# Performance work log

Hardware: AMD Instinct MI355X
Metric: run time of the kernel (lower is better)

## Reference

```python
import jax, jax.numpy as jnp
import numpy as np

N, G, S = 51200, 128, 400  # nodes, graphs, nodes-per-graph
E, IN, H, OUT = 819200, 128, 128, 10


def _graph_conv(x, src, dst, W_rel, b_rel, W_root):
    # PyG GraphConv (aggr='add'): lin_rel(sum_{j->i} x_j) + lin_root(x_i)
    agg = jax.ops.segment_sum(x[src], dst, num_segments=N)  # [N, d]
    return agg @ W_rel + b_rel + x @ W_root


def _mixup(x, lam, perm):
    return x * lam + (1.0 - lam) * x[perm]


def setup_inputs() -> dict:
    key = jax.random.key(0)
    ks = jax.random.split(key, 12)
    rng = np.random.default_rng(0)

    x0 = jax.random.normal(ks[0], (N, IN), dtype=jnp.float32)
    edge_index = jax.random.randint(ks[1], (2, E), 0, N, dtype=jnp.int64)
    lam = jax.random.uniform(ks[2], (1,), dtype=jnp.float32)
    ptr = jnp.arange(0, N + 1, S, dtype=jnp.int64)            # [G+1]
    batch = jnp.repeat(jnp.arange(G, dtype=jnp.int64), S)     # [N]

    def seg_perm():
        return jnp.asarray(np.concatenate(
            [g * S + rng.permutation(S) for g in range(G)]), dtype=jnp.int64)

    perm1, perm2, perm3 = seg_perm(), seg_perm(), seg_perm()

    def lin(k, fan_in, fan_out):
        bound = 1.0 / np.sqrt(fan_in)
        return jax.random.uniform(k, (fan_in, fan_out), jnp.float32, -bound, bound)

    params = {
        'W1_rel': lin(ks[3], IN, H), 'b1_rel': jnp.zeros((H,), jnp.float32),
        'W1_root': lin(ks[4], IN, H),
        'W2_rel': lin(ks[5], H, H), 'b2_rel': jnp.zeros((H,), jnp.float32),
        'W2_root': lin(ks[6], H, H),
        'W_lin': lin(ks[7], H, OUT), 'b_lin': jnp.zeros((OUT,), jnp.float32),
    }
    return dict(x0=x0, edge_index=edge_index, lam=lam, ptr=ptr, batch=batch,
                perm1=perm1, perm2=perm2, perm3=perm3, **params)


def reference(x0, edge_index, lam, ptr, batch, perm1, perm2, perm3,
              W1_rel, b1_rel, W1_root, W2_rel, b2_rel, W2_root, W_lin, b_lin):
    src, dst = edge_index[0], edge_index[1]
    l = lam[0]

    x1 = jax.nn.relu(_graph_conv(x0, src, dst, W1_rel, b1_rel, W1_root))
    x1 = _mixup(x1, l, perm1)  # dropout p=0.4 is identity in eval mode

    x2 = jax.nn.relu(_graph_conv(x1, src, dst, W2_rel, b2_rel, W2_root))
    x2 = _mixup(x2, l, perm2)

    # NOTE: original forward reuses conv2 for the third layer (conv3 unused)
    x3 = jax.nn.relu(_graph_conv(x2, src, dst, W2_rel, b2_rel, W2_root))
    x3 = _mixup(x3, l, perm3)

    pooled = jax.ops.segment_sum(x3, batch, num_segments=G)  # [G, H]
    logits = pooled @ W_lin + b_lin                          # [G, OUT]
    return jax.nn.log_softmax(logits, axis=-1)
```

## Files before the change

### kernel.cpp

```cpp
#include <hip/hip_runtime.h>

#define N_NODES 51200
#define N_EDGES 819200
#define HDIM 128
#define AK 256
#define NGRAPH 128
#define SEG 400
#define NOUT 10
#define SLOT 64

#define HISTW (N_NODES / 4)
#define NBLK 200
#define EPB (N_EDGES / NBLK)
#define SEGS 8
#define BPSEG (NBLK / SEGS)

typedef unsigned short ushort_t;
typedef unsigned int uint_t;
typedef __attribute__((ext_vector_type(8))) short bf16x8;
typedef __attribute__((ext_vector_type(16))) float f32x16;

static __device__ __forceinline__ unsigned short f2bf(float f) {
    unsigned int u = __float_as_uint(f);
    unsigned int r = (u + 0x7fffu + ((u >> 16) & 1u)) >> 16;
    return (unsigned short)r;
}
static __device__ __forceinline__ float bf2f(unsigned short h) {
    return __uint_as_float(((unsigned int)h) << 16);
}


__global__ void k_prep(const float* __restrict__ x, ushort_t* __restrict__ Abuf,
                       const float* __restrict__ W1rel, const float* __restrict__ W1root,
                       const float* __restrict__ W2rel, const float* __restrict__ W2root,
                       ushort_t* __restrict__ Wfrag1, ushort_t* __restrict__ Wfrag2,
                       float* __restrict__ pooled) {
    int b = blockIdx.x;
    if (b < 6400) {
        int idx = b * 256 + threadIdx.x;
        int row = idx >> 5;
        int c4 = (idx & 31) * 4;
        float4 v = *(const float4*)(x + (size_t)row * HDIM + c4);
        ushort4 h;
        h.x = f2bf(v.x); h.y = f2bf(v.y); h.z = f2bf(v.z); h.w = f2bf(v.w);
        *(ushort4*)(Abuf + (size_t)row * AK + HDIM + c4) = h;
    } else if (b < 6656) {
        int w2 = (b >= 6528);
        int tid = (b - (w2 ? 6528 : 6400)) * 256 + threadIdx.x;
        const float* Wrel  = w2 ? W2rel : W1rel;
        const float* Wroot = w2 ? W2root : W1root;
        ushort_t* dstF     = w2 ? Wfrag2 : Wfrag1;
        int j = tid & 7;
        int l = (tid >> 3) & 63;
        int s = (tid >> 9) & 15;
        int t = tid >> 13;
        int k = 16 * s + (l >> 5) * 8 + j;
        int n = 32 * t + (l & 31);
        float v = (k < HDIM) ? Wrel[(size_t)k * HDIM + n]
                             : Wroot[(size_t)(k - HDIM) * HDIM + n];
        dstF[tid] = f2bf(v);
    } else {
        int i = (b - 6656) * 256 + threadIdx.x;
        pooled[i] = 0.f;
    }
}


__global__ __launch_bounds__(256) void k_count(const int* __restrict__ dst,
                                               uint_t* __restrict__ bh) {
    __shared__ uint_t hist[HISTW];
    int b = blockIdx.x, tid = threadIdx.x;
    for (int i = tid; i < HISTW; i += 256) hist[i] = 0u;
    __syncthreads();
    const int4* d4 = (const int4*)dst + b * (EPB / 4);
#pragma unroll
    for (int p = 0; p < 4; ++p) {
        int4 d = d4[p * 256 + tid];
        atomicAdd(&hist[((uint_t)d.x) >> 2], 1u << ((d.x & 3) * 8));
        atomicAdd(&hist[((uint_t)d.y) >> 2], 1u << ((d.y & 3) * 8));
        atomicAdd(&hist[((uint_t)d.z) >> 2], 1u << ((d.z & 3) * 8));
        atomicAdd(&hist[((uint_t)d.w) >> 2], 1u << ((d.w & 3) * 8));
    }
    __syncthreads();
    for (int i = tid; i < HISTW; i += 256) bh[(size_t)b * HISTW + i] = hist[i];
}


__global__ __launch_bounds__(256) void k_prefix(uint_t* __restrict__ bh,
                                                int* __restrict__ cnt) {
    __shared__ uint_t segsum[SEGS][32];
    int ci = threadIdx.x & 31;
    int seg = threadIdx.x >> 5;
    int c = blockIdx.x * 32 + ci;
    uint_t v[BPSEG];
    uint_t sum = 0;
#pragma unroll
    for (int k = 0; k < BPSEG; ++k) {
        v[k] = bh[(size_t)(seg * BPSEG + k) * HISTW + c];
        sum += v[k];
    }
    segsum[seg][ci] = sum;
    __syncthreads();
    uint_t run = 0;
    for (int s = 0; s < seg; ++s) run += segsum[s][ci];
#pragma unroll
    for (int k = 0; k < BPSEG; ++k) {
        bh[(size_t)(seg * BPSEG + k) * HISTW + c] = run;
        run += v[k];
    }
    if (seg == SEGS - 1) {
        int4 o;
        o.x = (int)(run & 0xffu);
        o.y = (int)((run >> 8) & 0xffu);
        o.z = (int)((run >> 16) & 0xffu);
        o.w = (int)((run >> 24) & 0xffu);
        *(int4*)(cnt + 4 * c) = o;
    }
}


__global__ __launch_bounds__(256) void k_place(const int* __restrict__ src,
                                               const int* __restrict__ dst,
                                               const uint_t* __restrict__ bh,
                                               ushort_t* __restrict__ col2) {
    __shared__ uint_t hist[HISTW];
    int b = blockIdx.x, tid = threadIdx.x;
    for (int i = tid; i < HISTW; i += 256) hist[i] = bh[(size_t)b * HISTW + i];
    __syncthreads();
    const int4* d4 = (const int4*)dst + b * (EPB / 4);
    const int4* s4 = (const int4*)src + b * (EPB / 4);
#pragma unroll
    for (int p = 0; p < 4; ++p) {
        int4 d = d4[p * 256 + tid];
        int4 s = s4[p * 256 + tid];
#define PLACE1(dd, ss)                                                        \
        do {                                                                  \
            uint_t w = (uint_t)(dd);                                          \
            int sh = (int)(w & 3u) * 8;                                       \
            uint_t old = atomicAdd(&hist[w >> 2], 1u << sh);                  \
            col2[(size_t)w * SLOT + ((old >> sh) & 0xffu)] = (ushort_t)(ss);  \
        } while (0)
        PLACE1(d.x, s.x);
        PLACE1(d.y, s.y);
        PLACE1(d.z, s.z);
        PLACE1(d.w, s.w);
#undef PLACE1
    }
}


__global__ __launch_bounds__(256) void k_aggregate(ushort_t* __restrict__ Abuf,
                                                   const int* __restrict__ cnt,
                                                   const ushort_t* __restrict__ col) {
    int wave = threadIdx.x >> 6;
    int lane = threadIdx.x & 63;
    int il = lane & 15;
    int qe = lane >> 4;
    int node = blockIdx.x * 4 + wave;
    int beg = node * SLOT;
    int end = beg + cnt[node];

    const ushort_t* xsrc = Abuf + HDIM + (size_t)il * 8;

    float a[4][8];
#pragma unroll
    for (int j = 0; j < 4; ++j)
#pragma unroll
        for (int k = 0; k < 8; ++k) a[j][k] = 0.f;

    int e = beg;
    for (; e + 16 <= end; e += 16) {
        int c[4];
#pragma unroll
        for (int j = 0; j < 4; ++j) c[j] = (int)col[e + 4 * j + qe];
#pragma unroll
        for (int j = 0; j < 4; ++j) {
            uint4 v = *(const uint4*)(xsrc + (size_t)c[j] * AK);
            a[j][0] += __uint_as_float(v.x << 16);
            a[j][1] += __uint_as_float(v.x & 0xffff0000u);
            a[j][2] += __uint_as_float(v.y << 16);
            a[j][3] += __uint_as_float(v.y & 0xffff0000u);
            a[j][4] += __uint_as_float(v.z << 16);
            a[j][5] += __uint_as_float(v.z & 0xffff0000u);
            a[j][6] += __uint_as_float(v.w << 16);
            a[j][7] += __uint_as_float(v.w & 0xffff0000u);
        }
    }
    for (; e + 4 <= end; e += 4) {
        int c = (int)col[e + qe];
        uint4 v = *(const uint4*)(xsrc + (size_t)c * AK);
        a[0][0] += __uint_as_float(v.x << 16);
        a[0][1] += __uint_as_float(v.x & 0xffff0000u);
        a[0][2] += __uint_as_float(v.y << 16);
        a[0][3] += __uint_as_float(v.y & 0xffff0000u);
        a[0][4] += __uint_as_float(v.z << 16);
        a[0][5] += __uint_as_float(v.z & 0xffff0000u);
        a[0][6] += __uint_as_float(v.w << 16);
        a[0][7] += __uint_as_float(v.w & 0xffff0000u);
    }
    if (e < end) {
        int idx = e + qe;
        bool ok = idx < end;
        int c = (int)col[ok ? idx : e];
        uint4 v = *(const uint4*)(xsrc + (size_t)c * AK);
        a[1][0] += ok ? __uint_as_float(v.x << 16) : 0.f;
        a[1][1] += ok ? __uint_as_float(v.x & 0xffff0000u) : 0.f;
        a[1][2] += ok ? __uint_as_float(v.y << 16) : 0.f;
        a[1][3] += ok ? __uint_as_float(v.y & 0xffff0000u) : 0.f;
        a[1][4] += ok ? __uint_as_float(v.z << 16) : 0.f;
        a[1][5] += ok ? __uint_as_float(v.z & 0xffff0000u) : 0.f;
        a[1][6] += ok ? __uint_as_float(v.w << 16) : 0.f;
        a[1][7] += ok ? __uint_as_float(v.w & 0xffff0000u) : 0.f;
    }

    float s[8];
#pragma unroll
    for (int k = 0; k < 8; ++k) {
        s[k] = (a[0][k] + a[1][k]) + (a[2][k] + a[3][k]);
        s[k] += __shfl_xor(s[k], 16);
        s[k] += __shfl_xor(s[k], 32);
    }

    if (qe == 0) {
        uint4 o;
        o.x = (uint_t)f2bf(s[0]) | ((uint_t)f2bf(s[1]) << 16);
        o.y = (uint_t)f2bf(s[2]) | ((uint_t)f2bf(s[3]) << 16);
        o.z = (uint_t)f2bf(s[4]) | ((uint_t)f2bf(s[5]) << 16);
        o.w = (uint_t)f2bf(s[6]) | ((uint_t)f2bf(s[7]) << 16);
        *(uint4*)(Abuf + (size_t)node * AK + il * 8) = o;
    }
}


__global__ __launch_bounds__(64) void k_gemm_mfma(const ushort_t* __restrict__ Abuf,
                                                  const ushort_t* __restrict__ Wfrag,
                                                  const float* __restrict__ bias,
                                                  ushort_t* __restrict__ y) {
    __shared__ ushort_t sm[32][72];
    int lane = threadIdx.x;
    int nh = blockIdx.x & 1;
    int row0 = (blockIdx.x >> 1) * 32;
    int m = lane & 31;
    int half = lane >> 5;

    f32x16 acc[2];
#pragma unroll
    for (int t = 0; t < 2; ++t) acc[t] = (f32x16)(0.f);

    float bb[2];
#pragma unroll
    for (int t = 0; t < 2; ++t) bb[t] = bias[nh * 64 + t * 32 + m];

    const ushort_t* arow = Abuf + (size_t)(row0 + m) * AK + half * 8;
    const ushort_t* wf = Wfrag + (size_t)lane * 8 + (size_t)nh * 2 * 16 * 512;

#pragma unroll
    for (int s = 0; s < 16; ++s) {
        bf16x8 afrag = *(const bf16x8*)(arow + s * 16);
#pragma unroll
        for (int t = 0; t < 2; ++t) {
            bf16x8 bfrag = *(const bf16x8*)(wf + (size_t)(t * 16 + s) * 512);
            acc[t] = __builtin_amdgcn_mfma_f32_32x32x16_bf16(afrag, bfrag, acc[t], 0, 0, 0);
        }
    }

#pragma unroll
    for (int t = 0; t < 2; ++t) {
#pragma unroll
        for (int r = 0; r < 16; ++r) {
            int rowL = (r & 3) + 8 * (r >> 2) + 4 * half;
            sm[rowL][t * 32 + m] = f2bf(fmaxf(acc[t][r] + bb[t], 0.f));
        }
    }
    __syncthreads();
    int seg = lane & 7;
    int rbase = lane >> 3;
#pragma unroll
    for (int it = 0; it < 4; ++it) {
        int rowL = rbase + it * 8;
        int4 chunk = *(const int4*)&sm[rowL][seg * 8];
        *(int4*)(y + (size_t)(row0 + rowL) * HDIM + nh * 64 + seg * 8) = chunk;
    }
}


__global__ __launch_bounds__(64) void k_gemm_pool(const ushort_t* __restrict__ Abuf,
                                                  const ushort_t* __restrict__ Wfrag,
                                                  const float* __restrict__ bias,
                                                  float* __restrict__ pooled) {
    int lane = threadIdx.x;
    int nh = blockIdx.x & 1;
    int row0 = (blockIdx.x >> 1) * 32;
    int m = lane & 31;
    int half = lane >> 5;

    f32x16 acc[2];
#pragma unroll
    for (int t = 0; t < 2; ++t) acc[t] = (f32x16)(0.f);

    float bb[2];
#pragma unroll
    for (int t = 0; t < 2; ++t) bb[t] = bias[nh * 64 + t * 32 + m];

    const ushort_t* arow = Abuf + (size_t)(row0 + m) * AK + half * 8;
    const ushort_t* wf = Wfrag + (size_t)lane * 8 + (size_t)nh * 2 * 16 * 512;

#pragma unroll
    for (int s = 0; s < 16; ++s) {
        bf16x8 afrag = *(const bf16x8*)(arow + s * 16);
#pragma unroll
        for (int t = 0; t < 2; ++t) {
            bf16x8 bfrag = *(const bf16x8*)(wf + (size_t)(t * 16 + s) * 512);
            acc[t] = __builtin_amdgcn_mfma_f32_32x32x16_bf16(afrag, bfrag, acc[t], 0, 0, 0);
        }
    }

    int g0 = row0 / SEG;
    int bnd = (g0 + 1) * SEG;
    int straddle = (row0 + 31 >= bnd);

#pragma unroll
    for (int t = 0; t < 2; ++t) {
        float s0 = 0.f, s1 = 0.f;
#pragma unroll
        for (int r = 0; r < 16; ++r) {
            int row = row0 + (r & 3) + 8 * (r >> 2) + 4 * half;
            float v = fmaxf(acc[t][r] + bb[t], 0.f);
            if (row < bnd) s0 += v; else s1 += v;
        }
        s0 += __shfl_xor(s0, 32);
        s1 += __shfl_xor(s1, 32);
        if (half == 0) {
            int coln = nh * 64 + t * 32 + m;
            atomicAdd(&pooled[g0 * HDIM + coln], s0);
            if (straddle) atomicAdd(&pooled[(g0 + 1) * HDIM + coln], s1);
        }
    }
}


__global__ void k_mixup_toA(const ushort_t* __restrict__ y, const int* __restrict__ perm,
                            const float* __restrict__ lam, ushort_t* __restrict__ Abuf) {
    int idx = blockIdx.x * 256 + threadIdx.x;
    int row = idx >> 5;
    int c4 = (idx & 31) * 4;
    float l = lam[0];
    float om = 1.f - l;
    int p = perm[row];
    ushort4 a = *(const ushort4*)(y + (size_t)row * HDIM + c4);
    ushort4 b = *(const ushort4*)(y + (size_t)p * HDIM + c4);
    ushort4 o;
    o.x = f2bf(l * bf2f(a.x) + om * bf2f(b.x));
    o.y = f2bf(l * bf2f(a.y) + om * bf2f(b.y));
    o.z = f2bf(l * bf2f(a.z) + om * bf2f(b.z));
    o.w = f2bf(l * bf2f(a.w) + om * bf2f(b.w));
    *(ushort4*)(Abuf + (size_t)row * AK + HDIM + c4) = o;
}


__global__ __launch_bounds__(64) void k_final(const float* __restrict__ pooled,
                                              const float* __restrict__ Wlin,
                                              const float* __restrict__ blin,
                                              float* __restrict__ out) {
    int g = blockIdx.x;
    int lane = threadIdx.x;
    float2 v = *(const float2*)(pooled + (size_t)g * HDIM + lane * 2);
    float p[NOUT];
#pragma unroll
    for (int o = 0; o < NOUT; ++o)
        p[o] = v.x * Wlin[(size_t)(2 * lane) * NOUT + o] +
               v.y * Wlin[(size_t)(2 * lane + 1) * NOUT + o];
#pragma unroll
    for (int mask = 1; mask < 64; mask <<= 1)
#pragma unroll
        for (int o = 0; o < NOUT; ++o) p[o] += __shfl_xor(p[o], mask);
    if (lane == 0) {
        float lg[NOUT];
        float mx = -1e30f;
#pragma unroll
        for (int o = 0; o < NOUT; ++o) { lg[o] = p[o] + blin[o]; mx = fmaxf(mx, lg[o]); }
        float se = 0.f;
#pragma unroll
        for (int o = 0; o < NOUT; ++o) se += expf(lg[o] - mx);
        float lse = mx + logf(se);
#pragma unroll
        for (int o = 0; o < NOUT; ++o) out[g * NOUT + o] = lg[o] - lse;
    }
}


extern "C" void kernel_launch(void* const* d_in, const int* in_sizes, int n_in,
                              void* d_out, int out_size, void* d_ws, size_t ws_size,
                              hipStream_t stream) {
    const float* x0     = (const float*)d_in[0];
    const int*   edge   = (const int*)d_in[1];
    const int*   src    = edge;
    const int*   dst    = edge + N_EDGES;
    const float* lam    = (const float*)d_in[2];
    const int*   perm1  = (const int*)d_in[5];
    const int*   perm2  = (const int*)d_in[6];
    const float* W1_rel = (const float*)d_in[8];
    const float* b1_rel = (const float*)d_in[9];
    const float* W1_root= (const float*)d_in[10];
    const float* W2_rel = (const float*)d_in[11];
    const float* b2_rel = (const float*)d_in[12];
    const float* W2_root= (const float*)d_in[13];
    const float* W_lin  = (const float*)d_in[14];
    const float* b_lin  = (const float*)d_in[15];
    float* out = (float*)d_out;

    char* w = (char*)d_ws;
    size_t off = 0;
    auto alloc = [&](size_t bytes) -> void* {
        void* p = w + off;
        off = (off + bytes + 255) & ~(size_t)255;
        return p;
    };
    int* cnt       = (int*)alloc((size_t)N_NODES * 4);
    ushort_t* col2 = (ushort_t*)alloc((size_t)N_NODES * SLOT * 2);
    ushort_t* Abuf   = (ushort_t*)alloc((size_t)N_NODES * AK * 2);
    ushort_t* ybuf   = (ushort_t*)alloc((size_t)N_NODES * HDIM * 2);
    ushort_t* Wfrag1 = (ushort_t*)alloc(32768 * 2);
    ushort_t* Wfrag2 = (ushort_t*)alloc(32768 * 2);
    float* pooled    = (float*)alloc((size_t)NGRAPH * HDIM * 4);

    uint_t* bh = (uint_t*)ybuf;

    k_prep<<<6720, 256, 0, stream>>>(x0, Abuf, W1_rel, W1_root, W2_rel, W2_root,
                                     Wfrag1, Wfrag2, pooled);
    k_count<<<NBLK, 256, 0, stream>>>(dst, bh);
    k_prefix<<<HISTW / 32, 256, 0, stream>>>(bh, cnt);
    k_place<<<NBLK, 256, 0, stream>>>(src, dst, bh, col2);

    const int aggGrid  = N_NODES / 4;
    const int gemmGrid = (N_NODES / 32) * 2;
    const int elGrid   = (N_NODES * HDIM / 4) / 256;

    k_aggregate<<<aggGrid, 256, 0, stream>>>(Abuf, cnt, col2);
    k_gemm_mfma<<<gemmGrid, 64, 0, stream>>>(Abuf, Wfrag1, b1_rel, ybuf);
    k_mixup_toA<<<elGrid, 256, 0, stream>>>(ybuf, perm1, lam, Abuf);
    k_aggregate<<<aggGrid, 256, 0, stream>>>(Abuf, cnt, col2);
    k_gemm_mfma<<<gemmGrid, 64, 0, stream>>>(Abuf, Wfrag2, b2_rel, ybuf);
    k_mixup_toA<<<elGrid, 256, 0, stream>>>(ybuf, perm2, lam, Abuf);
    k_aggregate<<<aggGrid, 256, 0, stream>>>(Abuf, cnt, col2);
    k_gemm_pool<<<gemmGrid, 64, 0, stream>>>(Abuf, Wfrag2, b2_rel, pooled);

    k_final<<<NGRAPH, 64, 0, stream>>>(pooled, W_lin, b_lin, out);
}
```

Measured before the change: 279.7 us.

## Fuse neighbor aggregation and MFMA GEMM into one per-layer kernel via LDS

Aggregation and the dense GEMM are merged into a single kernel per layer. Each 256-thread block gathers 32 nodes' neighbor sums into an LDS tile alongside the root features, then runs MFMA over it, with each wave covering 32 output columns. This removes the round trip of aggregated rows through global memory and one launch per layer, and it shrinks the feature buffer from 256 to 128 columns. In exchange, each block now does serial per-node aggregation across its waves and holds a larger LDS tile, which may lower occupancy and latency hiding during the gather.

Result: slower. 298.8 us (+6.8%).

```diff
diff --git a/kernel.cpp b/kernel.cpp
--- a/kernel.cpp
+++ b/kernel.cpp
@@ -3,7 +3,6 @@
 #define N_NODES 51200
 #define N_EDGES 819200
 #define HDIM 128
-#define AK 256
 #define NGRAPH 128
 #define SEG 400
 #define NOUT 10
@@ -15,6 +14,8 @@
 #define SEGS 8
 #define BPSEG (NBLK / SEGS)
 
+#define LDSW 264
+
 typedef unsigned short ushort_t;
 typedef unsigned int uint_t;
 typedef __attribute__((ext_vector_type(8))) short bf16x8;
@@ -30,7 +31,7 @@
 }
 
 
-__global__ void k_prep(const float* __restrict__ x, ushort_t* __restrict__ Abuf,
+__global__ void k_prep(const float* __restrict__ x, ushort_t* __restrict__ xbuf,
                        const float* __restrict__ W1rel, const float* __restrict__ W1root,
                        const float* __restrict__ W2rel, const float* __restrict__ W2root,
                        ushort_t* __restrict__ Wfrag1, ushort_t* __restrict__ Wfrag2,
@@ -43,7 +44,7 @@
         float4 v = *(const float4*)(x + (size_t)row * HDIM + c4);
         ushort4 h;
         h.x = f2bf(v.x); h.y = f2bf(v.y); h.z = f2bf(v.z); h.w = f2bf(v.w);
-        *(ushort4*)(Abuf + (size_t)row * AK + HDIM + c4) = h;
+        *(ushort4*)(xbuf + (size_t)row * HDIM + c4) = h;
     } else if (b < 6656) {
         int w2 = (b >= 6528);
         int tid = (b - (w2 ? 6528 : 6400)) * 256 + threadIdx.x;
@@ -149,189 +150,150 @@
 }
 
 
-__global__ __launch_bounds__(256) void k_aggregate(ushort_t* __restrict__ Abuf,
-                                                   const int* __restrict__ cnt,
-                                                   const ushort_t* __restrict__ col) {
-    int wave = threadIdx.x >> 6;
-    int lane = threadIdx.x & 63;
+template<int POOL>
+__global__ __launch_bounds__(256) void k_layer(const ushort_t* __restrict__ xbuf,
+                                               const int* __restrict__ cnt,
+                                               const ushort_t* __restrict__ col,
+                                               const ushort_t* __restrict__ Wfrag,
+                                               const float* __restrict__ bias,
+                                               ushort_t* __restrict__ y,
+                                               float* __restrict__ pooled) {
+    __shared__ ushort_t At[32][LDSW];
+    int tid = threadIdx.x;
+    int w = tid >> 6;
+    int lane = tid & 63;
     int il = lane & 15;
     int qe = lane >> 4;
-    int node = blockIdx.x * 4 + wave;
-    int beg = node * SLOT;
-    int end = beg + cnt[node];
-
-    const ushort_t* xsrc = Abuf + HDIM + (size_t)il * 8;
-
-    float a[4][8];
-#pragma unroll
-    for (int j = 0; j < 4; ++j)
-#pragma unroll
-        for (int k = 0; k < 8; ++k) a[j][k] = 0.f;
-
-    int e = beg;
-    for (; e + 16 <= end; e += 16) {
-        int c[4];
-#pragma unroll
-        for (int j = 0; j < 4; ++j) c[j] = (int)col[e + 4 * j + qe];
-#pragma unroll
-        for (int j = 0; j < 4; ++j) {
-            uint4 v = *(const uint4*)(xsrc + (size_t)c[j] * AK);
-            a[j][0] += __uint_as_float(v.x << 16);
-            a[j][1] += __uint_as_float(v.x & 0xffff0000u);
-            a[j][2] += __uint_as_float(v.y << 16);
-            a[j][3] += __uint_as_float(v.y & 0xffff0000u);
-            a[j][4] += __uint_as_float(v.z << 16);
-            a[j][5] += __uint_as_float(v.z & 0xffff0000u);
-            a[j][6] += __uint_as_float(v.w << 16);
-            a[j][7] += __uint_as_float(v.w & 0xffff0000u);
-        }
-    }
-    for (; e + 4 <= end; e += 4) {
-        int c = (int)col[e + qe];
-        uint4 v = *(const uint4*)(xsrc + (size_t)c * AK);
-        a[0][0] += __uint_as_float(v.x << 16);
-        a[0][1] += __uint_as_float(v.x & 0xffff0000u);
-        a[0][2] += __uint_as_float(v.y << 16);
-        a[0][3] += __uint_as_float(v.y & 0xffff0000u);
-        a[0][4] += __uint_as_float(v.z << 16);
-        a[0][5] += __uint_as_float(v.z & 0xffff0000u);
-        a[0][6] += __uint_as_float(v.w << 16);
-        a[0][7] += __uint_as_float(v.w & 0xffff0000u);
-    }
-    if (e < end) {
-        int idx = e + qe;
-        bool ok = idx < end;
-        int c = (int)col[ok ? idx : e];
-        uint4 v = *(const uint4*)(xsrc + (size_t)c * AK);
-        a[1][0] += ok ? __uint_as_float(v.x << 16) : 0.f;
-        a[1][1] += ok ? __uint_as_float(v.x & 0xffff0000u) : 0.f;
-        a[1][2] += ok ? __uint_as_float(v.y << 16) : 0.f;
-        a[1][3] += ok ? __uint_as_float(v.y & 0xffff0000u) : 0.f;
-        a[1][4] += ok ? __uint_as_float(v.z << 16) : 0.f;
-        a[1][5] += ok ? __uint_as_float(v.z & 0xffff0000u) : 0.f;
-        a[1][6] += ok ? __uint_as_float(v.w << 16) : 0.f;
-        a[1][7] += ok ? __uint_as_float(v.w & 0xffff0000u) : 0.f;
-    }
-
-    float s[8];
-#pragma unroll
-    for (int k = 0; k < 8; ++k) {
-        s[k] = (a[0][k] + a[1][k]) + (a[2][k] + a[3][k]);
-        s[k] += __shfl_xor(s[k], 16);
-        s[k] += __shfl_xor(s[k], 32);
-    }
-
-    if (qe == 0) {
-        uint4 o;
-        o.x = (uint_t)f2bf(s[0]) | ((uint_t)f2bf(s[1]) << 16);
-        o.y = (uint_t)f2bf(s[2]) | ((uint_t)f2bf(s[3]) << 16);
-        o.z = (uint_t)f2bf(s[4]) | ((uint_t)f2bf(s[5]) << 16);
-        o.w = (uint_t)f2bf(s[6]) | ((uint_t)f2bf(s[7]) << 16);
-        *(uint4*)(Abuf + (size_t)node * AK + il * 8) = o;
-    }
-}
-
-
-__global__ __launch_bounds__(64) void k_gemm_mfma(const ushort_t* __restrict__ Abuf,
-                                                  const ushort_t* __restrict__ Wfrag,
-                                                  const float* __restrict__ bias,
-                                                  ushort_t* __restrict__ y) {
-    __shared__ ushort_t sm[32][72];
-    int lane = threadIdx.x;
-    int nh = blockIdx.x & 1;
-    int row0 = (blockIdx.x >> 1) * 32;
+    int row0 = blockIdx.x * 32;
+
+#pragma unroll
+    for (int p = 0; p < 2; ++p) {
+        int rl = w * 8 + p * 4 + qe;
+        uint4 v = *(const uint4*)(xbuf + (size_t)(row0 + rl) * HDIM + il * 8);
+        *(uint4*)&At[rl][HDIM + il * 8] = v;
+    }
+
+    const ushort_t* xsrc = xbuf + (size_t)il * 8;
+    for (int i = 0; i < 8; ++i) {
+        int rl = w * 8 + i;
+        int node = row0 + rl;
+        int beg = node * SLOT;
+        int end = beg + cnt[node];
+
+        float a[4][8];
+#pragma unroll
+        for (int j = 0; j < 4; ++j)
+#pragma unroll
+            for (int k = 0; k < 8; ++k) a[j][k] = 0.f;
+
+        int e = beg;
+        for (; e + 16 <= end; e += 16) {
+            int c[4];
+#pragma unroll
+            for (int j = 0; j < 4; ++j) c[j] = (int)col[e + 4 * j + qe];
+#pragma unroll
+            for (int j = 0; j < 4; ++j) {
+                uint4 v = *(const uint4*)(xsrc + (size_t)c[j] * HDIM);
+                a[j][0] += __uint_as_float(v.x << 16);
+                a[j][1] += __uint_as_float(v.x & 0xffff0000u);
+                a[j][2] += __uint_as_float(v.y << 16);
+                a[j][3] += __uint_as_float(v.y & 0xffff0000u);
+                a[j][4] += __uint_as_float(v.z << 16);
+                a[j][5] += __uint_as_float(v.z & 0xffff0000u);
+                a[j][6] += __uint_as_float(v.w << 16);
+                a[j][7] += __uint_as_float(v.w & 0xffff0000u);
+            }
+        }
+        for (; e + 4 <= end; e += 4) {
+            int c = (int)col[e + qe];
+            uint4 v = *(const uint4*)(xsrc + (size_t)c * HDIM);
+            a[0][0] += __uint_as_float(v.x << 16);
+            a[0][1] += __uint_as_float(v.x & 0xffff0000u);
+            a[0][2] += __uint_as_float(v.y << 16);
+            a[0][3] += __uint_as_float(v.y & 0xffff0000u);
+            a[0][4] += __uint_as_float(v.z << 16);
+            a[0][5] += __uint_as_float(v.z & 0xffff0000u);
+            a[0][6] += __uint_as_float(v.w << 16);
+            a[0][7] += __uint_as_float(v.w & 0xffff0000u);
+        }
+        if (e < end) {
+            int idx = e + qe;
+            bool ok = idx < end;
+            int c = (int)col[ok ? idx : e];
+            uint4 v = *(const uint4*)(xsrc + (size_t)c * HDIM);
+            a[1][0] += ok ? __uint_as_float(v.x << 16) : 0.f;
+            a[1][1] += ok ? __uint_as_float(v.x & 0xffff0000u) : 0.f;
+            a[1][2] += ok ? __uint_as_float(v.y << 16) : 0.f;
+            a[1][3] += ok ? __uint_as_float(v.y & 0xffff0000u) : 0.f;
+            a[1][4] += ok ? __uint_as_float(v.z << 16) : 0.f;
+            a[1][5] += ok ? __uint_as_float(v.z & 0xffff0000u) : 0.f;
+            a[1][6] += ok ? __uint_as_float(v.w << 16) : 0.f;
+            a[1][7] += ok ? __uint_as_float(v.w & 0xffff0000u) : 0.f;
+        }
+
+        float s[8];
+#pragma unroll
+        for (int k = 0; k < 8; ++k) {
+            s[k] = (a[0][k] + a[1][k]) + (a[2][k] + a[3][k]);
+            s[k] += __shfl_xor(s[k], 16);
+            s[k] += __shfl_xor(s[k], 32);
+        }
+
+        if (qe == 0) {
+            uint4 o;
+            o.x = (uint_t)f2bf(s[0]) | ((uint_t)f2bf(s[1]) << 16);
+            o.y = (uint_t)f2bf(s[2]) | ((uint_t)f2bf(s[3]) << 16);
+            o.z = (uint_t)f2bf(s[4]) | ((uint_t)f2bf(s[5]) << 16);
+            o.w = (uint_t)f2bf(s[6]) | ((uint_t)f2bf(s[7]) << 16);
+            *(uint4*)&At[rl][il * 8] = o;
+        }
+    }
+    __syncthreads();
+
     int m = lane & 31;
     int half = lane >> 5;
-
-    f32x16 acc[2];
-#pragma unroll
-    for (int t = 0; t < 2; ++t) acc[t] = (f32x16)(0.f);
-
-    float bb[2];
-#pragma unroll
-    for (int t = 0; t < 2; ++t) bb[t] = bias[nh * 64 + t * 32 + m];
-
-    const ushort_t* arow = Abuf + (size_t)(row0 + m) * AK + half * 8;
-    const ushort_t* wf = Wfrag + (size_t)lane * 8 + (size_t)nh * 2 * 16 * 512;
+    f32x16 acc = (f32x16)(0.f);
+    float bb = bias[w * 32 + m];
+    const ushort_t* arow = &At[m][half * 8];
+    const ushort_t* wf = Wfrag + (size_t)lane * 8;
 
 #pragma unroll
     for (int s = 0; s < 16; ++s) {
         bf16x8 afrag = *(const bf16x8*)(arow + s * 16);
-#pragma unroll
-        for (int t = 0; t < 2; ++t) {
-            bf16x8 bfrag = *(const bf16x8*)(wf + (size_t)(t * 16 + s) * 512);
-            acc[t] = __builtin_amdgcn_mfma_f32_32x32x16_bf16(afrag, bfrag, acc[t], 0, 0, 0);
-        }
-    }
-
-#pragma unroll
-    for (int t = 0; t < 2; ++t) {
+        bf16x8 bfrag = *(const bf16x8*)(wf + (size_t)(w * 16 + s) * 512);
+        acc = __builtin_amdgcn_mfma_f32_32x32x16_bf16(afrag, bfrag, acc, 0, 0, 0);
+    }
+
+    if (POOL == 0) {
+        __syncthreads();
 #pragma unroll
         for (int r = 0; r < 16; ++r) {
             int rowL = (r & 3) + 8 * (r >> 2) + 4 * half;
-            sm[rowL][t * 32 + m] = f2bf(fmaxf(acc[t][r] + bb[t], 0.f));
-        }
-    }
-    __syncthreads();
-    int seg = lane & 7;
-    int rbase = lane >> 3;
-#pragma unroll
-    for (int it = 0; it < 4; ++it) {
-        int rowL = rbase + it * 8;
-        int4 chunk = *(const int4*)&sm[rowL][seg * 8];
-        *(int4*)(y + (size_t)(row0 + rowL) * HDIM + nh * 64 + seg * 8) = chunk;
-    }
-}
-
-
-__global__ __launch_bounds__(64) void k_gemm_pool(const ushort_t* __restrict__ Abuf,
-                                                  const ushort_t* __restrict__ Wfrag,
-                                                  const float* __restrict__ bias,
-                                                  float* __restrict__ pooled) {
-    int lane = threadIdx.x;
-    int nh = blockIdx.x & 1;
-    int row0 = (blockIdx.x >> 1) * 32;
-    int m = lane & 31;
-    int half = lane >> 5;
-
-    f32x16 acc[2];
-#pragma unroll
-    for (int t = 0; t < 2; ++t) acc[t] = (f32x16)(0.f);
-
-    float bb[2];
-#pragma unroll
-    for (int t = 0; t < 2; ++t) bb[t] = bias[nh * 64 + t * 32 + m];
-
-    const ushort_t* arow = Abuf + (size_t)(row0 + m) * AK + half * 8;
-    const ushort_t* wf = Wfrag + (size_t)lane * 8 + (size_t)nh * 2 * 16 * 512;
-
-#pragma unroll
-    for (int s = 0; s < 16; ++s) {
-        bf16x8 afrag = *(const bf16x8*)(arow + s * 16);
-#pragma unroll
-        for (int t = 0; t < 2; ++t) {
-            bf16x8 bfrag = *(const bf16x8*)(wf + (size_t)(t * 16 + s) * 512);
-            acc[t] = __builtin_amdgcn_mfma_f32_32x32x16_bf16(afrag, bfrag, acc[t], 0, 0, 0);
-        }
-    }
-
-    int g0 = row0 / SEG;
-    int bnd = (g0 + 1) * SEG;
-    int straddle = (row0 + 31 >= bnd);
-
-#pragma unroll
-    for (int t = 0; t < 2; ++t) {
+            At[rowL][w * 32 + m] = f2bf(fmaxf(acc[r] + bb, 0.f));
+        }
+        __syncthreads();
+#pragma unroll
+        for (int it = 0; it < 2; ++it) {
+            int c = it * 256 + tid;
+            int row = c >> 4;
+            int sg = c & 15;
+            *(int4*)(y + (size_t)(row0 + row) * HDIM + sg * 8) = *(const int4*)&At[row][sg * 8];
+        }
+    } else {
+        int g0 = row0 / SEG;
+        int bnd = (g0 + 1) * SEG;
+        int straddle = (row0 + 31 >= bnd);
         float s0 = 0.f, s1 = 0.f;
 #pragma unroll
         for (int r = 0; r < 16; ++r) {
             int row = row0 + (r & 3) + 8 * (r >> 2) + 4 * half;
-            float v = fmaxf(acc[t][r] + bb[t], 0.f);
+            float v = fmaxf(acc[r] + bb, 0.f);
             if (row < bnd) s0 += v; else s1 += v;
         }
         s0 += __shfl_xor(s0, 32);
         s1 += __shfl_xor(s1, 32);
         if (half == 0) {
-            int coln = nh * 64 + t * 32 + m;
+            int coln = w * 32 + m;
             atomicAdd(&pooled[g0 * HDIM + coln], s0);
             if (straddle) atomicAdd(&pooled[(g0 + 1) * HDIM + coln], s1);
         }
@@ -340,7 +302,7 @@
 
 
 __global__ void k_mixup_toA(const ushort_t* __restrict__ y, const int* __restrict__ perm,
-                            const float* __restrict__ lam, ushort_t* __restrict__ Abuf) {
+                            const float* __restrict__ lam, ushort_t* __restrict__ xbuf) {
     int idx = blockIdx.x * 256 + threadIdx.x;
     int row = idx >> 5;
     int c4 = (idx & 31) * 4;
@@ -354,7 +316,7 @@
     o.y = f2bf(l * bf2f(a.y) + om * bf2f(b.y));
     o.z = f2bf(l * bf2f(a.z) + om * bf2f(b.z));
     o.w = f2bf(l * bf2f(a.w) + om * bf2f(b.w));
-    *(ushort4*)(Abuf + (size_t)row * AK + HDIM + c4) = o;
+    *(ushort4*)(xbuf + (size_t)row * HDIM + c4) = o;
 }
 
 
@@ -418,7 +380,7 @@
     };
     int* cnt       = (int*)alloc((size_t)N_NODES * 4);
     ushort_t* col2 = (ushort_t*)alloc((size_t)N_NODES * SLOT * 2);
-    ushort_t* Abuf   = (ushort_t*)alloc((size_t)N_NODES * AK * 2);
+    ushort_t* xbuf   = (ushort_t*)alloc((size_t)N_NODES * HDIM * 2);
     ushort_t* ybuf   = (ushort_t*)alloc((size_t)N_NODES * HDIM * 2);
     ushort_t* Wfrag1 = (ushort_t*)alloc(32768 * 2);
     ushort_t* Wfrag2 = (ushort_t*)alloc(32768 * 2);
@@ -426,24 +388,20 @@
 
     uint_t* bh = (uint_t*)ybuf;
 
-    k_prep<<<6720, 256, 0, stream>>>(x0, Abuf, W1_rel, W1_root, W2_rel, W2_root,
+    k_prep<<<6720, 256, 0, stream>>>(x0, xbuf, W1_rel, W1_root, W2_rel, W2_root,
                                      Wfrag1, Wfrag2, pooled);
     k_count<<<NBLK, 256, 0, stream>>>(dst, bh);
     k_prefix<<<HISTW / 32, 256, 0, stream>>>(bh, cnt);
     k_place<<<NBLK, 256, 0, stream>>>(src, dst, bh, col2);
 
-    const int aggGrid  = N_NODES / 4;
-    const int gemmGrid = (N_NODES / 32) * 2;
-    const int elGrid   = (N_NODES * HDIM / 4) / 256;
-
-    k_aggregate<<<aggGrid, 256, 0, stream>>>(Abuf, cnt, col2);
-    k_gemm_mfma<<<gemmGrid, 64, 0, stream>>>(Abuf, Wfrag1, b1_rel, ybuf);
-    k_mixup_toA<<<elGrid, 256, 0, stream>>>(ybuf, perm1, lam, Abuf);
-    k_aggregate<<<aggGrid, 256, 0, stream>>>(Abuf, cnt, col2);
-    k_gemm_mfma<<<gemmGrid, 64, 0, stream>>>(Abuf, Wfrag2, b2_rel, ybuf);
-    k_mixup_toA<<<elGrid, 256, 0, stream>>>(ybuf, perm2, lam, Abuf);
-    k_aggregate<<<aggGrid, 256, 0, stream>>>(Abuf, cnt, col2);
-    k_gemm_pool<<<gemmGrid, 64, 0, stream>>>(Abuf, Wfrag2, b2_rel, pooled);
+    const int layGrid = N_NODES / 32;
+    const int elGrid  = (N_NODES * HDIM / 4) / 256;
+
+    k_layer<0><<<layGrid, 256, 0, stream>>>(xbuf, cnt, col2, Wfrag1, b1_rel, ybuf, pooled);
+    k_mixup_toA<<<elGrid, 256, 0, stream>>>(ybuf, perm1, lam, xbuf);
+    k_layer<0><<<layGrid, 256, 0, stream>>>(xbuf, cnt, col2, Wfrag2, b2_rel, ybuf, pooled);
+    k_mixup_toA<<<elGrid, 256, 0, stream>>>(ybuf, perm2, lam, xbuf);
+    k_layer<1><<<layGrid, 256, 0, stream>>>(xbuf, cnt, col2, Wfrag2, b2_rel, ybuf, pooled);
 
     k_final<<<NGRAPH, 64, 0, stream>>>(pooled, W_lin, b_lin, out);
 }
```
